# Kernel optimization log

Hardware: AMD Instinct MI355X
Metric: run time of the kernel (lower is better)

## Reference

```python
import jax, jax.numpy as jnp
import numpy as np

DIM = 1024
HEADS = 16
GROUPS = 4
DIM_HEAD = 64
INNER = HEADS * DIM_HEAD  # 1024
KV_DIM = 2 * DIM_HEAD * GROUPS  # 512
B, N = 4, 2048
EPS = 1e-6


def _layernorm(x, scale, bias, eps=EPS):
    mu = jnp.mean(x, axis=-1, keepdims=True)
    var = jnp.mean(jnp.square(x - mu), axis=-1, keepdims=True)
    return (x - mu) * jax.lax.rsqrt(var + eps) * scale + bias


def setup_inputs() -> dict:
    key = jax.random.key(0)
    ks = jax.random.split(key, 10)
    lecun = lambda k, shape: jax.random.normal(k, shape, jnp.float32) * (1.0 / np.sqrt(shape[0]))
    return {
        "x": jax.random.normal(ks[0], (B, N, DIM), jnp.float32),
        "ln_scale": jnp.ones((DIM,), jnp.float32),
        "ln_bias": jnp.zeros((DIM,), jnp.float32),
        "Wq": lecun(ks[1], (DIM, INNER)),
        "Wkv": lecun(ks[2], (DIM, KV_DIM)),
        "qn_scale": jnp.ones((DIM_HEAD,), jnp.float32),
        "qn_bias": jnp.zeros((DIM_HEAD,), jnp.float32),
        "kn_scale": jnp.ones((DIM_HEAD,), jnp.float32),
        "kn_bias": jnp.zeros((DIM_HEAD,), jnp.float32),
        "Wout": lecun(ks[3], (INNER, DIM)),
    }


def reference(x, ln_scale, ln_bias, Wq, Wkv, qn_scale, qn_bias, kn_scale, kn_bias, Wout):
    b, n, _ = x.shape
    g, hg, d = GROUPS, HEADS // GROUPS, DIM_HEAD
    scale = d ** -0.5
    xn = _layernorm(x, ln_scale, ln_bias)
    # q: (b,n,inner) -> (b,h,n,d)
    q = (xn @ Wq).reshape(b, n, HEADS, d).transpose(0, 2, 1, 3)
    kv = xn @ Wkv
    k, v = jnp.split(kv, 2, axis=-1)
    # (b,n,g*d) -> (b,g,n,d)
    k = k.reshape(b, n, g, d).transpose(0, 2, 1, 3)
    v = v.reshape(b, n, g, d).transpose(0, 2, 1, 3)
    q = _layernorm(q, qn_scale, qn_bias)
    k = _layernorm(k, kn_scale, kn_bias)
    # split heads into groups: (b, g*hg, n, d) -> (b, g, hg, n, d)
    qg = q.reshape(b, g, hg, n, d)
    dots = jnp.einsum('bghqd,bgkd->bghqk', qg, k) * scale
    attn = jax.nn.softmax(dots, axis=-1)
    out = jnp.einsum('bghqk,bgkd->bghqd', attn, v)  # (b,g,hg,n,d)
    out = out.transpose(0, 3, 1, 2, 4).reshape(b, n, g * hg * d)
    return out @ Wout
```

## Files before the change

kernel.cpp:

```cpp
#include <hip/hip_runtime.h>
#include <cstdint>
#include <cstddef>

typedef unsigned short u16;
typedef __attribute__((ext_vector_type(4))) float f32x4;
typedef __attribute__((ext_vector_type(8))) __bf16 bf16x8;
typedef __attribute__((ext_vector_type(4))) __bf16 bf16x4;
typedef __attribute__((ext_vector_type(8))) unsigned short u16x8;
typedef __attribute__((ext_vector_type(4))) unsigned short u16x4;

#define DEV static __device__ __forceinline__

#if __has_builtin(__builtin_amdgcn_exp2f)
#define EXP2(x) __builtin_amdgcn_exp2f(x)
#else
#define EXP2(x) exp2f(x)
#endif

DEV float bf2f(u16 v) { return __uint_as_float(((unsigned)v) << 16); }
DEV u16 f2bf(float f) {
  unsigned u = __float_as_uint(f);
  return (u16)((u + 0x7FFFu + ((u >> 16) & 1u)) >> 16);
}

DEV void gl_lds16(const void* g, void* l) {
  __builtin_amdgcn_global_load_lds((const __attribute__((address_space(1))) void*)g,
                                   (__attribute__((address_space(3))) void*)l, 16, 0, 0);
}

__global__ __launch_bounds__(256) void transpose64(const float* __restrict__ in,
                                                   u16* __restrict__ out, int incols) {
  __shared__ __attribute__((aligned(16))) u16 t[64 * 72];
  const int r0 = blockIdx.x * 64, c0 = blockIdx.y * 64, tid = threadIdx.x;
#pragma unroll
  for (int i = 0; i < 2; i++) {
    int c = i * 256 + tid;
    int row = c >> 3, cc = c & 7;
    const float* src = &in[(size_t)(r0 + row) * incols + c0 + cc * 8];
    f32x4 v0 = *(const f32x4*)src;
    f32x4 v1 = *(const f32x4*)(src + 4);
    u16x8 o;
#pragma unroll
    for (int j = 0; j < 4; j++) { o[j] = f2bf(v0[j]); o[4 + j] = f2bf(v1[j]); }
    *(u16x8*)&t[row * 72 + cc * 8] = o;
  }
  __syncthreads();
#pragma unroll
  for (int i = 0; i < 2; i++) {
    int c = i * 256 + tid;
    int d = c >> 3, nc = c & 7;
    u16x8 o;
#pragma unroll
    for (int j = 0; j < 8; j++) o[j] = t[(nc * 8 + j) * 72 + d];
    *(u16x8*)&out[(size_t)(c0 + d) * 1024 + r0 + nc * 8] = o;
  }
}

__global__ __launch_bounds__(256) void ln_x(const float* __restrict__ x,
                                            const float* __restrict__ sc,
                                            const float* __restrict__ bi,
                                            u16* __restrict__ xn) {
  __shared__ float red[8];
  const int row = blockIdx.x, tid = threadIdx.x;
  const int w = tid >> 6;
  f32x4 f = *(const f32x4*)&x[(size_t)row * 1024 + tid * 4];
  float s = f[0] + f[1] + f[2] + f[3];
  float q = f[0] * f[0] + f[1] * f[1] + f[2] * f[2] + f[3] * f[3];
#pragma unroll
  for (int off = 1; off < 64; off <<= 1) {
    s += __shfl_xor(s, off);
    q += __shfl_xor(q, off);
  }
  if ((tid & 63) == 0) { red[w] = s; red[4 + w] = q; }
  __syncthreads();
  float S = red[0] + red[1] + red[2] + red[3];
  float Q = red[4] + red[5] + red[6] + red[7];
  float mu = S * (1.0f / 1024.0f);
  float var = Q * (1.0f / 1024.0f) - mu * mu;
  float rs = rsqrtf(var + 1e-6f);
  f32x4 scv = *(const f32x4*)&sc[tid * 4];
  f32x4 biv = *(const f32x4*)&bi[tid * 4];
  u16* o = xn + (size_t)row * 1024 + tid * 4;
#pragma unroll
  for (int j = 0; j < 4; j++) o[j] = f2bf((f[j] - mu) * rs * scv[j] + biv[j]);
}

template <bool F32OUT>
__global__ __launch_bounds__(256) void gemm_bt(const u16* __restrict__ A,
                                               const u16* __restrict__ Bt,
                                               void* __restrict__ Cp,
                                               int M, int N, int K) {
  __shared__ __attribute__((aligned(16))) u16 Als[128 * 64];
  __shared__ __attribute__((aligned(16))) u16 Bls[128 * 64];
  const int tid = threadIdx.x;
  const int w = tid >> 6, lane = tid & 63, ln = lane & 15, quad = lane >> 4;
  const int m0 = blockIdx.y * 128, n0 = blockIdx.x * 128;
  const int moff = (w & 1) * 64, noff = (w >> 1) * 64;
  const f32x4 fzero = {0.f, 0.f, 0.f, 0.f};
  f32x4 acc[4][4];
#pragma unroll
  for (int i = 0; i < 4; i++)
#pragma unroll
    for (int j = 0; j < 4; j++) acc[i][j] = fzero;

  const u16* aS[4];
  const u16* bS[4];
#pragma unroll
  for (int i = 0; i < 4; i++) {
    int s = i * 256 + tid;
    int row = s >> 3, cs = (s & 7) ^ (row & 7);
    aS[i] = A + (size_t)(m0 + row) * K + cs * 8;
    bS[i] = Bt + (size_t)(n0 + row) * K + cs * 8;
  }

  for (int k0 = 0; k0 < K; k0 += 64) {
    __syncthreads();
#pragma unroll
    for (int i = 0; i < 4; i++) {
      int s = i * 256 + tid;
      gl_lds16(aS[i] + k0, &Als[s * 8]);
      gl_lds16(bS[i] + k0, &Bls[s * 8]);
    }
    __syncthreads();
#pragma unroll
    for (int kk = 0; kk < 2; kk++) {
      bf16x8 af[4], bfv[4];
#pragma unroll
      for (int mi = 0; mi < 4; mi++)
        af[mi] = *(const bf16x8*)
            &Als[(moff + mi * 16 + ln) * 64 + (((kk * 4 + quad) ^ (ln & 7)) * 8)];
#pragma unroll
      for (int ni = 0; ni < 4; ni++)
        bfv[ni] = *(const bf16x8*)
            &Bls[(noff + ni * 16 + ln) * 64 + (((kk * 4 + quad) ^ (ln & 7)) * 8)];
#pragma unroll
      for (int mi = 0; mi < 4; mi++)
#pragma unroll
        for (int ni = 0; ni < 4; ni++)
          acc[mi][ni] = __builtin_amdgcn_mfma_f32_16x16x32_bf16(af[mi], bfv[ni],
                                                                acc[mi][ni], 0, 0, 0);
    }
  }
#pragma unroll
  for (int mi = 0; mi < 4; mi++)
#pragma unroll
    for (int ni = 0; ni < 4; ni++)
#pragma unroll
      for (int r = 0; r < 4; r++) {
        size_t m = m0 + moff + mi * 16 + quad * 4 + r;
        size_t n = n0 + noff + ni * 16 + ln;
        if (F32OUT)
          ((float*)Cp)[m * N + n] = acc[mi][ni][r];
        else
          ((u16*)Cp)[m * N + n] = f2bf(acc[mi][ni][r]);
      }
}

__global__ __launch_bounds__(256) void qk_ln(const u16* __restrict__ qkv,
                                             const float* __restrict__ qs,
                                             const float* __restrict__ qb,
                                             const float* __restrict__ ks,
                                             const float* __restrict__ kb,
                                             u16* __restrict__ Q,
                                             u16* __restrict__ Kb) {
  const float SCL = 0.18033688011112042f;
  const int m = blockIdx.x;
  const int b = m >> 11, n = m & 2047;
  const int tid = threadIdx.x, w = tid >> 6, lane = tid & 63;
  const u16* rowp = qkv + (size_t)m * 1536;
  const float qsc = qs[lane], qbi = qb[lane];
  const float ksc = ks[lane], kbi = kb[lane];
#pragma unroll
  for (int i = 0; i < 4; i++) {
    int h = w * 4 + i;
    float v = bf2f(rowp[h * 64 + lane]);
    float s = v, q2 = v * v;
#pragma unroll
    for (int off = 1; off < 64; off <<= 1) {
      s += __shfl_xor(s, off);
      q2 += __shfl_xor(q2, off);
    }
    float mu = s * (1.0f / 64.0f);
    float var = q2 * (1.0f / 64.0f) - mu * mu;
    float y = ((v - mu) * rsqrtf(var + 1e-6f) * qsc + qbi) * SCL;
    Q[((size_t)(b * 16 + h) * 2048 + n) * 64 + lane] = f2bf(y);
  }
  {
    int g = w;
    float v = bf2f(rowp[1024 + g * 64 + lane]);
    float s = v, q2 = v * v;
#pragma unroll
    for (int off = 1; off < 64; off <<= 1) {
      s += __shfl_xor(s, off);
      q2 += __shfl_xor(q2, off);
    }
    float mu = s * (1.0f / 64.0f);
    float var = q2 * (1.0f / 64.0f) - mu * mu;
    float y = (v - mu) * rsqrtf(var + 1e-6f) * ksc + kbi;
    Kb[((size_t)(b * 4 + g) * 2048 + n) * 64 + lane] = f2bf(y);
  }
}

__global__ __launch_bounds__(256) void vtrans(const u16* __restrict__ qkv,
                                              u16* __restrict__ Vt) {
  __shared__ __attribute__((aligned(16))) u16 t[64 * 72];
  const int n0 = blockIdx.x * 64;
  const int bg = blockIdx.y;
  const int b = bg >> 2, g = bg & 3;
  const int tid = threadIdx.x;
  const u16* src = qkv + (size_t)(b * 2048 + n0) * 1536 + 1280 + g * 64;
#pragma unroll
  for (int i = 0; i < 2; i++) {
    int c = i * 256 + tid;
    int row = c >> 3, cc = c & 7;
    *(f32x4*)&t[row * 72 + cc * 8] = *(const f32x4*)&src[(size_t)row * 1536 + cc * 8];
  }
  __syncthreads();
  u16* dst = Vt + (size_t)bg * 64 * 2048 + n0;
#pragma unroll
  for (int i = 0; i < 2; i++) {
    int c = i * 256 + tid;
    int d = c >> 3, nc = c & 7;
    const int pA = 32 * (nc >> 2) + (nc & 1) * 16 + ((nc >> 1) & 1) * 4;
    u16x8 o;
#pragma unroll
    for (int j = 0; j < 8; j++) o[j] = t[(nc * 8 + j) * 72 + d];
    u16x4 lo = {o[0], o[1], o[2], o[3]};
    u16x4 hi = {o[4], o[5], o[6], o[7]};
    *(u16x4*)&dst[(size_t)d * 2048 + pA] = lo;
    *(u16x4*)&dst[(size_t)d * 2048 + pA + 8] = hi;
  }
}

__global__ __launch_bounds__(256, 4) void attn(const u16* __restrict__ Q,
                                               const u16* __restrict__ Kb,
                                               const u16* __restrict__ Vt,
                                               u16* __restrict__ Out) {
  __shared__ __attribute__((aligned(16))) u16 Kls0[64 * 64];
  __shared__ __attribute__((aligned(16))) u16 Kls1[64 * 64];
  __shared__ __attribute__((aligned(16))) u16 Vls0[64 * 64];
  __shared__ __attribute__((aligned(16))) u16 Vls1[64 * 64];
  const int qt = blockIdx.x;
  const int bh = blockIdx.y;
  const int b = bh >> 4, h = bh & 15, g = h >> 2;
  const int tid = threadIdx.x, w = tid >> 6, lane = tid & 63;
  const int ln = lane & 15, quad = lane >> 4;
  const u16* Qg = Q + ((size_t)(b * 16 + h) * 2048 + qt * 128 + w * 32) * 64;
  const u16* Kg = Kb + (size_t)(b * 4 + g) * 2048 * 64;
  const u16* Vg = Vt + (size_t)(b * 4 + g) * 64 * 2048;
  const f32x4 fzero = {0.f, 0.f, 0.f, 0.f};

  bf16x8 qf[2][2];
#pragma unroll
  for (int mi = 0; mi < 2; mi++)
#pragma unroll
    for (int ks2 = 0; ks2 < 2; ks2++)
      qf[mi][ks2] = *(const bf16x8*)&Qg[(size_t)(mi * 16 + ln) * 64 + ks2 * 32 + quad * 8];

  f32x4 oacc[4][2];
#pragma unroll
  for (int ni = 0; ni < 4; ni++)
#pragma unroll
    for (int mi = 0; mi < 2; mi++) oacc[ni][mi] = fzero;
  float lsum[2] = {0.f, 0.f};

  const int sk0 = tid, sk1 = 256 + tid;
  const int krow0 = sk0 >> 3, kcs0 = (sk0 & 7) ^ (krow0 & 7);
  const int krow1 = sk1 >> 3, kcs1 = (sk1 & 7) ^ (krow1 & 7);

  auto STAGE = [&](int kt, u16* Kd, u16* Vd) {
    gl_lds16(Kg + (size_t)(kt * 64 + krow0) * 64 + kcs0 * 8, &Kd[sk0 * 8]);
    gl_lds16(Kg + (size_t)(kt * 64 + krow1) * 64 + kcs1 * 8, &Kd[sk1 * 8]);
    gl_lds16(Vg + (size_t)krow0 * 2048 + kt * 64 + kcs0 * 8, &Vd[sk0 * 8]);
    gl_lds16(Vg + (size_t)krow1 * 2048 + kt * 64 + kcs1 * 8, &Vd[sk1 * 8]);
  };

  auto BODY = [&](int kt, const u16* K_, const u16* V_, u16* Kn, u16* Vn) {
    if (kt + 1 < 32) STAGE(kt + 1, Kn, Vn);

    f32x4 sacc[2][4];
#pragma unroll
    for (int ni = 0; ni < 4; ni++) {
      const int krow = ni * 16 + ln;
      bf16x8 kf0 = *(const bf16x8*)&K_[krow * 64 + ((quad ^ (ln & 7)) * 8)];
      bf16x8 kf1 = *(const bf16x8*)&K_[krow * 64 + (((4 + quad) ^ (ln & 7)) * 8)];
#pragma unroll
      for (int mi = 0; mi < 2; mi++) {
        f32x4 tt = __builtin_amdgcn_mfma_f32_16x16x32_bf16(kf0, qf[mi][0], fzero, 0, 0, 0);
        sacc[mi][ni] = __builtin_amdgcn_mfma_f32_16x16x32_bf16(kf1, qf[mi][1], tt, 0, 0, 0);
      }
    }

    bf16x8 pfa[2][2];
#pragma unroll
    for (int mi = 0; mi < 2; mi++) {
      float ls = 0.f;
#pragma unroll
      for (int ni = 0; ni < 4; ni++) {
        float p0 = EXP2(sacc[mi][ni][0]);
        float p1 = EXP2(sacc[mi][ni][1]);
        float p2 = EXP2(sacc[mi][ni][2]);
        float p3 = EXP2(sacc[mi][ni][3]);
        ls += (p0 + p1) + (p2 + p3);
        const int e = (ni & 1) * 4;
        pfa[mi][ni >> 1][e + 0] = (__bf16)p0;
        pfa[mi][ni >> 1][e + 1] = (__bf16)p1;
        pfa[mi][ni >> 1][e + 2] = (__bf16)p2;
        pfa[mi][ni >> 1][e + 3] = (__bf16)p3;
      }
      ls += __shfl_xor(ls, 16);
      ls += __shfl_xor(ls, 32);
      lsum[mi] += ls;
    }

#pragma unroll
    for (int kc = 0; kc < 2; kc++) {
#pragma unroll
      for (int ni = 0; ni < 4; ni++) {
        bf16x8 vf = *(const bf16x8*)
            &V_[(ni * 16 + ln) * 64 + (((4 * kc + quad) ^ (ln & 7)) * 8)];
#pragma unroll
        for (int mi = 0; mi < 2; mi++)
          oacc[ni][mi] = __builtin_amdgcn_mfma_f32_16x16x32_bf16(vf, pfa[mi][kc],
                                                                 oacc[ni][mi], 0, 0, 0);
      }
    }
    __syncthreads();
  };

  STAGE(0, Kls0, Vls0);
  __syncthreads();
  for (int kt = 0; kt < 32; kt += 2) {
    BODY(kt, Kls0, Vls0, Kls1, Vls1);
    BODY(kt + 1, Kls1, Vls1, Kls0, Vls0);
  }

#pragma unroll
  for (int mi = 0; mi < 2; mi++) {
    float inv = 1.0f / lsum[mi];
    u16* Og = Out + ((size_t)b * 2048 + qt * 128 + w * 32 + mi * 16 + ln) * 1024 + h * 64;
#pragma unroll
    for (int ni = 0; ni < 4; ni++) {
      bf16x4 ov = {(__bf16)(oacc[ni][mi][0] * inv), (__bf16)(oacc[ni][mi][1] * inv),
                   (__bf16)(oacc[ni][mi][2] * inv), (__bf16)(oacc[ni][mi][3] * inv)};
      *(bf16x4*)&Og[ni * 16 + quad * 4] = ov;
    }
  }
}

extern "C" void kernel_launch(void* const* d_in, const int* in_sizes, int n_in,
                              void* d_out, int out_size, void* d_ws, size_t ws_size,
                              hipStream_t stream) {
  const float* x    = (const float*)d_in[0];
  const float* lns  = (const float*)d_in[1];
  const float* lnb  = (const float*)d_in[2];
  const float* Wq   = (const float*)d_in[3];
  const float* Wkv  = (const float*)d_in[4];
  const float* qns  = (const float*)d_in[5];
  const float* qnb  = (const float*)d_in[6];
  const float* kns  = (const float*)d_in[7];
  const float* knb  = (const float*)d_in[8];
  const float* Wout = (const float*)d_in[9];
  float* out = (float*)d_out;
  char* ws = (char*)d_ws;

  const size_t o_xn  = 0;
  const size_t o_qkv = 16777216;
  const size_t o_bt  = o_qkv + 25165824;
  const size_t o_k   = o_bt + 3145728;
  const size_t o_vt  = o_k + 4194304;
  u16* xn   = (u16*)(ws + o_xn);
  u16* qkv  = (u16*)(ws + o_qkv);
  u16* bt   = (u16*)(ws + o_bt);
  u16* Kbuf = (u16*)(ws + o_k);
  u16* Vtb  = (u16*)(ws + o_vt);
  u16* Qbuf = xn;
  u16* aout = qkv;

  transpose64<<<dim3(16, 16), 256, 0, stream>>>(Wq, bt, 1024);
  transpose64<<<dim3(16, 8), 256, 0, stream>>>(Wkv, bt + 1024 * 1024, 512);
  ln_x<<<8192, 256, 0, stream>>>(x, lns, lnb, xn);
  gemm_bt<false><<<dim3(12, 64), 256, 0, stream>>>(xn, bt, qkv, 8192, 1536, 1024);
  transpose64<<<dim3(16, 16), 256, 0, stream>>>(Wout, bt, 1024);
  qk_ln<<<8192, 256, 0, stream>>>(qkv, qns, qnb, kns, knb, Qbuf, Kbuf);
  vtrans<<<dim3(32, 16), 256, 0, stream>>>(qkv, Vtb);
  attn<<<dim3(16, 64), 256, 0, stream>>>(Qbuf, Kbuf, Vtb, aout);
  gemm_bt<true><<<dim3(8, 64), 256, 0, stream>>>(aout, bt, out, 8192, 1024, 1024);

  (void)in_sizes; (void)n_in; (void)out_size; (void)ws_size;
}
```

Measured before the change: 276.4 us.

## Give each attention wave 64 query rows with 2 waves per block

The attention kernel now runs 128 threads (2 waves) per block, and each wave handles 64 query rows instead of 32. This reuses each K/V fragment read from LDS across four MFMA row tiles rather than two. The score computation is split into two 32-key chunks so the softmax and PV steps can interleave with it. Row-sum shuffles move out of the inner loop to the epilogue, and s_setprio is wrapped around the MFMA bursts. The cost is higher register pressure, lower occupancy (launch bounds drop to 128,2), and each thread staging twice as many K/V loads.

New measurement: 272.3 us. About the same (-1.5%).

```diff
diff --git a/kernel.cpp b/kernel.cpp
--- a/kernel.cpp
+++ b/kernel.cpp
@@ -232,7 +232,7 @@
   }
 }
 
-__global__ __launch_bounds__(256, 4) void attn(const u16* __restrict__ Q,
+__global__ __launch_bounds__(128, 2) void attn(const u16* __restrict__ Q,
                                                const u16* __restrict__ Kb,
                                                const u16* __restrict__ Vt,
                                                u16* __restrict__ Out) {
@@ -245,84 +245,96 @@
   const int b = bh >> 4, h = bh & 15, g = h >> 2;
   const int tid = threadIdx.x, w = tid >> 6, lane = tid & 63;
   const int ln = lane & 15, quad = lane >> 4;
-  const u16* Qg = Q + ((size_t)(b * 16 + h) * 2048 + qt * 128 + w * 32) * 64;
+  const u16* Qg = Q + ((size_t)(b * 16 + h) * 2048 + qt * 128 + w * 64) * 64;
   const u16* Kg = Kb + (size_t)(b * 4 + g) * 2048 * 64;
   const u16* Vg = Vt + (size_t)(b * 4 + g) * 64 * 2048;
   const f32x4 fzero = {0.f, 0.f, 0.f, 0.f};
 
-  bf16x8 qf[2][2];
-#pragma unroll
-  for (int mi = 0; mi < 2; mi++)
+  bf16x8 qf[4][2];
+#pragma unroll
+  for (int mi = 0; mi < 4; mi++)
 #pragma unroll
     for (int ks2 = 0; ks2 < 2; ks2++)
       qf[mi][ks2] = *(const bf16x8*)&Qg[(size_t)(mi * 16 + ln) * 64 + ks2 * 32 + quad * 8];
 
-  f32x4 oacc[4][2];
+  f32x4 oacc[4][4];
 #pragma unroll
   for (int ni = 0; ni < 4; ni++)
 #pragma unroll
-    for (int mi = 0; mi < 2; mi++) oacc[ni][mi] = fzero;
-  float lsum[2] = {0.f, 0.f};
-
-  const int sk0 = tid, sk1 = 256 + tid;
-  const int krow0 = sk0 >> 3, kcs0 = (sk0 & 7) ^ (krow0 & 7);
-  const int krow1 = sk1 >> 3, kcs1 = (sk1 & 7) ^ (krow1 & 7);
+    for (int mi = 0; mi < 4; mi++) oacc[ni][mi] = fzero;
+  float lacc[4] = {0.f, 0.f, 0.f, 0.f};
+
+  int krow[4], kcs[4];
+#pragma unroll
+  for (int i = 0; i < 4; i++) {
+    int s = i * 128 + tid;
+    krow[i] = s >> 3;
+    kcs[i] = (s & 7) ^ (krow[i] & 7);
+  }
 
   auto STAGE = [&](int kt, u16* Kd, u16* Vd) {
-    gl_lds16(Kg + (size_t)(kt * 64 + krow0) * 64 + kcs0 * 8, &Kd[sk0 * 8]);
-    gl_lds16(Kg + (size_t)(kt * 64 + krow1) * 64 + kcs1 * 8, &Kd[sk1 * 8]);
-    gl_lds16(Vg + (size_t)krow0 * 2048 + kt * 64 + kcs0 * 8, &Vd[sk0 * 8]);
-    gl_lds16(Vg + (size_t)krow1 * 2048 + kt * 64 + kcs1 * 8, &Vd[sk1 * 8]);
+#pragma unroll
+    for (int i = 0; i < 4; i++) {
+      int s = i * 128 + tid;
+      gl_lds16(Kg + (size_t)(kt * 64 + krow[i]) * 64 + kcs[i] * 8, &Kd[s * 8]);
+      gl_lds16(Vg + (size_t)krow[i] * 2048 + kt * 64 + kcs[i] * 8, &Vd[s * 8]);
+    }
   };
 
   auto BODY = [&](int kt, const u16* K_, const u16* V_, u16* Kn, u16* Vn) {
     if (kt + 1 < 32) STAGE(kt + 1, Kn, Vn);
 
-    f32x4 sacc[2][4];
-#pragma unroll
-    for (int ni = 0; ni < 4; ni++) {
-      const int krow = ni * 16 + ln;
-      bf16x8 kf0 = *(const bf16x8*)&K_[krow * 64 + ((quad ^ (ln & 7)) * 8)];
-      bf16x8 kf1 = *(const bf16x8*)&K_[krow * 64 + (((4 + quad) ^ (ln & 7)) * 8)];
-#pragma unroll
-      for (int mi = 0; mi < 2; mi++) {
-        f32x4 tt = __builtin_amdgcn_mfma_f32_16x16x32_bf16(kf0, qf[mi][0], fzero, 0, 0, 0);
-        sacc[mi][ni] = __builtin_amdgcn_mfma_f32_16x16x32_bf16(kf1, qf[mi][1], tt, 0, 0, 0);
+#pragma unroll
+    for (int c = 0; c < 2; c++) {
+      bf16x8 kf[2][2];
+#pragma unroll
+      for (int ni = 0; ni < 2; ni++) {
+        const int kr = (c * 32 + ni * 16 + ln) * 64;
+        kf[ni][0] = *(const bf16x8*)&K_[kr + ((quad ^ (ln & 7)) * 8)];
+        kf[ni][1] = *(const bf16x8*)&K_[kr + (((4 + quad) ^ (ln & 7)) * 8)];
       }
-    }
-
-    bf16x8 pfa[2][2];
-#pragma unroll
-    for (int mi = 0; mi < 2; mi++) {
-      float ls = 0.f;
-#pragma unroll
-      for (int ni = 0; ni < 4; ni++) {
-        float p0 = EXP2(sacc[mi][ni][0]);
-        float p1 = EXP2(sacc[mi][ni][1]);
-        float p2 = EXP2(sacc[mi][ni][2]);
-        float p3 = EXP2(sacc[mi][ni][3]);
-        ls += (p0 + p1) + (p2 + p3);
-        const int e = (ni & 1) * 4;
-        pfa[mi][ni >> 1][e + 0] = (__bf16)p0;
-        pfa[mi][ni >> 1][e + 1] = (__bf16)p1;
-        pfa[mi][ni >> 1][e + 2] = (__bf16)p2;
-        pfa[mi][ni >> 1][e + 3] = (__bf16)p3;
+
+      f32x4 sacc[4][2];
+      __builtin_amdgcn_s_setprio(1);
+#pragma unroll
+      for (int ni = 0; ni < 2; ni++)
+#pragma unroll
+        for (int mi = 0; mi < 4; mi++) {
+          f32x4 tt = __builtin_amdgcn_mfma_f32_16x16x32_bf16(kf[ni][0], qf[mi][0],
+                                                             fzero, 0, 0, 0);
+          sacc[mi][ni] = __builtin_amdgcn_mfma_f32_16x16x32_bf16(kf[ni][1], qf[mi][1],
+                                                                 tt, 0, 0, 0);
+        }
+      __builtin_amdgcn_s_setprio(0);
+
+      bf16x8 pfa[4];
+#pragma unroll
+      for (int mi = 0; mi < 4; mi++) {
+        float p0 = EXP2(sacc[mi][0][0]);
+        float p1 = EXP2(sacc[mi][0][1]);
+        float p2 = EXP2(sacc[mi][0][2]);
+        float p3 = EXP2(sacc[mi][0][3]);
+        float p4 = EXP2(sacc[mi][1][0]);
+        float p5 = EXP2(sacc[mi][1][1]);
+        float p6 = EXP2(sacc[mi][1][2]);
+        float p7 = EXP2(sacc[mi][1][3]);
+        lacc[mi] += ((p0 + p1) + (p2 + p3)) + ((p4 + p5) + (p6 + p7));
+        pfa[mi][0] = (__bf16)p0; pfa[mi][1] = (__bf16)p1;
+        pfa[mi][2] = (__bf16)p2; pfa[mi][3] = (__bf16)p3;
+        pfa[mi][4] = (__bf16)p4; pfa[mi][5] = (__bf16)p5;
+        pfa[mi][6] = (__bf16)p6; pfa[mi][7] = (__bf16)p7;
       }
-      ls += __shfl_xor(ls, 16);
-      ls += __shfl_xor(ls, 32);
-      lsum[mi] += ls;
-    }
-
-#pragma unroll
-    for (int kc = 0; kc < 2; kc++) {
+
 #pragma unroll
       for (int ni = 0; ni < 4; ni++) {
         bf16x8 vf = *(const bf16x8*)
-            &V_[(ni * 16 + ln) * 64 + (((4 * kc + quad) ^ (ln & 7)) * 8)];
-#pragma unroll
-        for (int mi = 0; mi < 2; mi++)
-          oacc[ni][mi] = __builtin_amdgcn_mfma_f32_16x16x32_bf16(vf, pfa[mi][kc],
+            &V_[(ni * 16 + ln) * 64 + (((4 * c + quad) ^ (ln & 7)) * 8)];
+        __builtin_amdgcn_s_setprio(1);
+#pragma unroll
+        for (int mi = 0; mi < 4; mi++)
+          oacc[ni][mi] = __builtin_amdgcn_mfma_f32_16x16x32_bf16(vf, pfa[mi],
                                                                  oacc[ni][mi], 0, 0, 0);
+        __builtin_amdgcn_s_setprio(0);
       }
     }
     __syncthreads();
@@ -336,9 +348,12 @@
   }
 
 #pragma unroll
-  for (int mi = 0; mi < 2; mi++) {
-    float inv = 1.0f / lsum[mi];
-    u16* Og = Out + ((size_t)b * 2048 + qt * 128 + w * 32 + mi * 16 + ln) * 1024 + h * 64;
+  for (int mi = 0; mi < 4; mi++) {
+    float ls = lacc[mi];
+    ls += __shfl_xor(ls, 16);
+    ls += __shfl_xor(ls, 32);
+    float inv = 1.0f / ls;
+    u16* Og = Out + ((size_t)b * 2048 + qt * 128 + w * 64 + mi * 16 + ln) * 1024 + h * 64;
 #pragma unroll
     for (int ni = 0; ni < 4; ni++) {
       bf16x4 ov = {(__bf16)(oacc[ni][mi][0] * inv), (__bf16)(oacc[ni][mi][1] * inv),
@@ -384,7 +399,7 @@
   transpose64<<<dim3(16, 16), 256, 0, stream>>>(Wout, bt, 1024);
   qk_ln<<<8192, 256, 0, stream>>>(qkv, qns, qnb, kns, knb, Qbuf, Kbuf);
   vtrans<<<dim3(32, 16), 256, 0, stream>>>(qkv, Vtb);
-  attn<<<dim3(16, 64), 256, 0, stream>>>(Qbuf, Kbuf, Vtb, aout);
+  attn<<<dim3(16, 64), 128, 0, stream>>>(Qbuf, Kbuf, Vtb, aout);
   gemm_bt<true><<<dim3(8, 64), 256, 0, stream>>>(aout, bt, out, 8192, 1024, 1024);
 
   (void)in_sizes; (void)n_in; (void)out_size; (void)ws_size;
```
